# Performance work log

Measured on AMD Instinct MI355X. Metric: run time of the kernel, lower is better.

The kernel has to match this reference:

```python
import jax, jax.numpy as jnp
import numpy as np

ALPHA = 20.0 / 100.0  # dt / tau
ONE_MINUS_ALPHA = 1.0 - ALPHA


def setup_inputs() -> dict:
    key = jax.random.key(0)
    ks = jax.random.split(key, 7)
    T, B, I, H, O = 512, 256, 256, 1024, 128
    si, sh, so = 1.0 / np.sqrt(I), 1.0 / np.sqrt(H), 1.0 / np.sqrt(H)
    return {
        "x": jax.random.normal(ks[0], (T, B, I), dtype=jnp.float32),
        "Wi": jax.random.normal(ks[1], (H, I), dtype=jnp.float32) * si,
        "bi": jax.random.normal(ks[2], (H,), dtype=jnp.float32) * si,
        "Wh": jax.random.normal(ks[3], (H, H), dtype=jnp.float32) * sh,
        "bh": jax.random.normal(ks[4], (H,), dtype=jnp.float32) * sh,
        "Wo": jax.random.normal(ks[5], (O, H), dtype=jnp.float32) * so,
        "bo": jax.random.normal(ks[6], (O,), dtype=jnp.float32) * so,
    }


def reference(x, Wi, bi, Wh, bh, Wo, bo):
    T, B, I = x.shape
    H = Wh.shape[0]
    # Precompute input projection for all timesteps: [T, B, H]
    inp_proj = jnp.einsum("tbi,hi->tbh", x, Wi) + bi

    def step(carry, u_t):
        state, out = carry
        total = u_t + out @ Wh.T + bh
        state = state * ONE_MINUS_ALPHA + total * ALPHA
        out = jax.nn.relu(state)
        return (state, out), out

    init = (jnp.zeros((B, H), x.dtype), jnp.zeros((B, H), x.dtype))
    (_, _), rnn_activity = jax.lax.scan(step, init, inp_proj)  # [T, B, H]
    out = jnp.einsum("tbh,oh->tbo", rnn_activity, Wo) + bo  # [T, B, O]
    return out, rnn_activity
```

## Files before the change

### kernel.cpp

```cpp
#include <hip/hip_runtime.h>

using f4_t  = __attribute__((ext_vector_type(4))) float;
using bf8_t = __attribute__((ext_vector_type(8))) short;
using u32x4 = __attribute__((ext_vector_type(4))) unsigned int;

#define T_DIM 512
#define B_DIM 256
#define I_DIM 256
#define H_DIM 1024
#define O_DIM 128

#define SWZ(row, byte) ((byte) ^ (((row) & 7) << 4))
#define HSWZ(row, byte) ((byte) ^ (((row) & 15) << 4))

#define SMASK 0x8000800080008000ull

__device__ __forceinline__ unsigned short f2bf(float f) {
  unsigned u = __builtin_bit_cast(unsigned, f);
  return (unsigned short)((u + 0x7FFFu + ((u >> 16) & 1u)) >> 16);
}

__device__ __forceinline__ unsigned long long pack4bf(f4_t v) {
  unsigned long long r;
  r  = (unsigned long long)f2bf(v[0]);
  r |= (unsigned long long)f2bf(v[1]) << 16;
  r |= (unsigned long long)f2bf(v[2]) << 32;
  r |= (unsigned long long)f2bf(v[3]) << 48;
  return r;
}

__global__ __launch_bounds__(256, 1) void k_init(
    const float* __restrict__ Wi, const float* __restrict__ Wh,
    const float* __restrict__ Wo, unsigned short* __restrict__ Wi_b,
    unsigned short* __restrict__ Wh_b, unsigned short* __restrict__ Wo_b,
    unsigned short* __restrict__ hbuf1, unsigned* __restrict__ done) {
  int idx = blockIdx.x * 256 + threadIdx.x;
  int stride = gridDim.x * 256;
  for (int i = idx; i < H_DIM * H_DIM; i += stride) Wh_b[i] = f2bf(Wh[i]);
  for (int i = idx; i < H_DIM * I_DIM; i += stride) Wi_b[i] = f2bf(Wi[i]);
  for (int i = idx; i < O_DIM * H_DIM; i += stride) Wo_b[i] = f2bf(Wo[i]);
  for (int i = idx; i < B_DIM * H_DIM; i += stride) hbuf1[i] = 0x8000;
  for (int i = idx; i < 256 * 32; i += stride) done[i] = 0;
}

__global__ __launch_bounds__(256, 2) void k_inproj(
    const float* __restrict__ x, const unsigned short* __restrict__ Wi_b,
    const float* __restrict__ bi, float* __restrict__ act) {
  __shared__ unsigned short As[128 * 128];
  __shared__ unsigned short Bs[128 * 128];
  int blk = blockIdx.x;
  int mb = (blk & 7) * 128 + (blk >> 6);
  int nb = (blk >> 3) & 7;
  int m0 = mb * 128, n0 = nb * 128;
  int tid = threadIdx.x;
  int lane = tid & 63, w = tid >> 6;
  int wm0 = (w & 1) * 64, wn0 = (w >> 1) * 64;
  int lrow = lane & 15, lk = (lane >> 4) * 8;
  f4_t acc[4][4];
#pragma unroll
  for (int a = 0; a < 4; ++a)
#pragma unroll
    for (int b = 0; b < 4; ++b) acc[a][b] = (f4_t){0.f, 0.f, 0.f, 0.f};

  for (int kb = 0; kb < 2; ++kb) {
    if (kb) __syncthreads();
#pragma unroll
    for (int it = 0; it < 16; ++it) {
      int c = it * 256 + tid;
      int row = c >> 5;
      int kc = (c & 31) * 4;
      f4_t v = *(const f4_t*)(x + (size_t)(m0 + row) * I_DIM + kb * 128 + kc);
      *(unsigned long long*)((char*)As + SWZ(row, row * 256 + kc * 2)) = pack4bf(v);
    }
#pragma unroll
    for (int it = 0; it < 8; ++it) {
      int c = it * 256 + tid;
      int row = c >> 4;
      int k16 = c & 15;
      u32x4 v = *(const u32x4*)(Wi_b + (size_t)(n0 + row) * I_DIM + kb * 128 + k16 * 8);
      *(u32x4*)((char*)Bs + SWZ(row, row * 256 + k16 * 16)) = v;
    }
    __syncthreads();
#pragma unroll
    for (int ks = 0; ks < 4; ++ks) {
      bf8_t aF[4], bF[4];
#pragma unroll
      for (int mt = 0; mt < 4; ++mt) {
        int row = wm0 + mt * 16 + lrow;
        aF[mt] = *(const bf8_t*)((char*)As + SWZ(row, row * 256 + (ks * 32 + lk) * 2));
      }
#pragma unroll
      for (int nt = 0; nt < 4; ++nt) {
        int row = wn0 + nt * 16 + lrow;
        bF[nt] = *(const bf8_t*)((char*)Bs + SWZ(row, row * 256 + (ks * 32 + lk) * 2));
      }
#pragma unroll
      for (int mt = 0; mt < 4; ++mt)
#pragma unroll
        for (int nt = 0; nt < 4; ++nt)
          acc[mt][nt] =
              __builtin_amdgcn_mfma_f32_16x16x32_bf16(aF[mt], bF[nt], acc[mt][nt], 0, 0, 0);
    }
  }
#pragma unroll
  for (int nt = 0; nt < 4; ++nt) {
    int col = n0 + wn0 + nt * 16 + lrow;
    float bv = bi[col];
#pragma unroll
    for (int mt = 0; mt < 4; ++mt) {
      int rbase = m0 + wm0 + mt * 16 + (lane >> 4) * 4;
#pragma unroll
      for (int r = 0; r < 4; ++r)
        act[(size_t)(rbase + r) * H_DIM + col] = acc[mt][nt][r] + bv;
    }
  }
}

__global__ __launch_bounds__(512, 1) void k_scan(
    const unsigned short* __restrict__ Wh_b, const float* __restrict__ bh,
    float* __restrict__ act, unsigned short* __restrict__ hbuf0,
    unsigned short* __restrict__ hbuf1, unsigned* __restrict__ done) {
  __shared__ __align__(16) char hT[16 * 2048];
  __shared__ __align__(16) float pbuf[4][16][132];
  int blk = blockIdx.x;
  int g = blk & 15, hs = blk >> 4;
  int b0 = g * 16, h0 = hs * 128;
  int tid = threadIdx.x;
  int lane = tid & 63, w = tid >> 6;
  int nb = w & 1, ks = w >> 1;
  int lrow = lane & 15, lgq = lane >> 4;

  bf8_t Bf[4][8];
#pragma unroll
  for (int n = 0; n < 4; ++n)
#pragma unroll
    for (int kc = 0; kc < 8; ++kc)
      Bf[n][kc] = *(const bf8_t*)(Wh_b +
                                  (size_t)(h0 + nb * 64 + n * 16 + lrow) * H_DIM +
                                  ks * 256 + kc * 32 + lgq * 8);

  int pr = tid >> 5, pc = (tid & 31) * 4;
  float st[4] = {0.f, 0.f, 0.f, 0.f};
  f4_t bh4 = *(const f4_t*)(bh + h0 + pc);

  unsigned short* hb[2] = {hbuf0, hbuf1};
  unsigned* myslot = done + (g * 8 + hs) * 32;
  const unsigned* pollp = done + (g * 8 + (lane & 7)) * 32;
  bool dopoll = (lane < 8) && (lane != hs);

  f4_t ucur = *(const f4_t*)(act + (size_t)(b0 + pr) * H_DIM + h0 + pc);

  for (int t = 0; t < T_DIM; ++t) {
    int p = t & 1;
    const unsigned short* hprev = hb[p ^ 1];
    unsigned want32 = ((((unsigned)(t - 1) >> 1) & 1u) ? 0x80008000u : 0u);

    if (t > 0 && dopoll) {
      int gd = 0;
      while (__hip_atomic_load(pollp, __ATOMIC_RELAXED, __HIP_MEMORY_SCOPE_AGENT) <
                 (unsigned)t &&
             ++gd < 60000)
        __builtin_amdgcn_s_sleep(1);
    }
    __builtin_amdgcn_sched_barrier(0);

    const char* base = (const char*)(hprev + (size_t)b0 * H_DIM);
    unsigned long long a0 = (unsigned long long)(base + tid * 16);
    u32x4 q0, q1, q2, q3;
    asm volatile(
        "global_load_dwordx4 %[d0], %[a0], off sc0 sc1\n\t"
        "global_load_dwordx4 %[d1], %[a1], off sc0 sc1\n\t"
        "global_load_dwordx4 %[d2], %[a2], off sc0 sc1\n\t"
        "global_load_dwordx4 %[d3], %[a3], off sc0 sc1\n\t"
        "s_waitcnt vmcnt(0)"
        : [d0] "=&v"(q0), [d1] "=&v"(q1), [d2] "=&v"(q2), [d3] "=&v"(q3)
        : [a0] "v"(a0), [a1] "v"(a0 + 8192), [a2] "v"(a0 + 16384),
          [a3] "v"(a0 + 24576)
        : "memory");
    __builtin_amdgcn_sched_barrier(0);

    int tn = (t + 1 < T_DIM) ? t + 1 : t;
    f4_t unext = *(const f4_t*)(act + ((size_t)tn * B_DIM + b0 + pr) * H_DIM + h0 + pc);

#define STALE(qq) \
  ((((qq[0] ^ want32) | (qq[1] ^ want32) | (qq[2] ^ want32) | (qq[3] ^ want32)) & \
    0x80008000u) != 0u)
#define RELOAD(qq, ad)                                                          \
  asm volatile("global_load_dwordx4 %0, %1, off sc0 sc1\n\ts_waitcnt vmcnt(0)"  \
               : "=&v"(qq)                                                      \
               : "v"(ad)                                                        \
               : "memory")
    {
      int vg = 0;
      for (;;) {
        unsigned m = (STALE(q0) ? 1u : 0u) | (STALE(q1) ? 2u : 0u) |
                     (STALE(q2) ? 4u : 0u) | (STALE(q3) ? 8u : 0u);
        if (m == 0u || ++vg >= 400) break;
        __builtin_amdgcn_s_sleep(1);
        if (m & 1u) RELOAD(q0, a0);
        if (m & 2u) RELOAD(q1, a0 + 8192);
        if (m & 4u) RELOAD(q2, a0 + 16384);
        if (m & 8u) RELOAD(q3, a0 + 24576);
      }
    }
#undef STALE
#undef RELOAD
#pragma unroll
    for (int d = 0; d < 4; ++d) {
      q0[d] &= 0x7fff7fffu; q1[d] &= 0x7fff7fffu;
      q2[d] &= 0x7fff7fffu; q3[d] &= 0x7fff7fffu;
    }

    int rh = tid >> 7;
    int colb = (tid & 127) * 16;
#define STAGE(qq, k)                                                            \
  *(u32x4*)(&hT[((k) * 4 + rh) * 2048 + HSWZ((k) * 4 + rh, colb)]) = qq
    STAGE(q0, 0); STAGE(q1, 1); STAGE(q2, 2); STAGE(q3, 3);
#undef STAGE
    asm volatile("s_waitcnt lgkmcnt(0)\ns_barrier" ::: "memory");
    __builtin_amdgcn_sched_barrier(0);

    f4_t acc[4];
#pragma unroll
    for (int n = 0; n < 4; ++n) acc[n] = (f4_t){0.f, 0.f, 0.f, 0.f};
#pragma unroll
    for (int kc = 0; kc < 8; ++kc) {
      int cbyte = ks * 512 + kc * 64 + lgq * 16;
      bf8_t Af = *(const bf8_t*)(&hT[lrow * 2048 + HSWZ(lrow, cbyte)]);
#pragma unroll
      for (int n = 0; n < 4; ++n)
        acc[n] = __builtin_amdgcn_mfma_f32_16x16x32_bf16(Af, Bf[n][kc], acc[n], 0, 0, 0);
    }

#pragma unroll
    for (int n = 0; n < 4; ++n)
#pragma unroll
      for (int r = 0; r < 4; ++r)
        pbuf[ks][lgq * 4 + r][nb * 64 + n * 16 + lrow] = acc[n][r];
    asm volatile("s_waitcnt lgkmcnt(0)\ns_barrier" ::: "memory");
    __builtin_amdgcn_sched_barrier(0);

    f4_t s0 = *(const f4_t*)&pbuf[0][pr][pc];
    f4_t s1 = *(const f4_t*)&pbuf[1][pr][pc];
    f4_t s2 = *(const f4_t*)&pbuf[2][pr][pc];
    f4_t s3 = *(const f4_t*)&pbuf[3][pr][pc];
    f4_t tot = s0 + s1 + s2 + s3 + ucur + bh4;
    f4_t hres;
#pragma unroll
    for (int j = 0; j < 4; ++j) {
      st[j] = st[j] * 0.8f + tot[j] * 0.2f;
      hres[j] = fmaxf(st[j], 0.f);
    }

    unsigned long long hp = pack4bf(hres) | (((t >> 1) & 1) ? SMASK : 0ull);
    unsigned long long sa =
        (unsigned long long)(hb[p] + (size_t)(b0 + pr) * H_DIM + h0 + pc);
    asm volatile("global_store_dwordx2 %0, %1, off sc0 sc1" ::"v"(sa), "v"(hp)
                 : "memory");

    asm volatile("s_barrier" ::: "memory");
    if (tid == 0)
      __hip_atomic_store(myslot, (unsigned)(t + 1), __ATOMIC_RELAXED,
                         __HIP_MEMORY_SCOPE_AGENT);

    *(f4_t*)(act + ((size_t)t * B_DIM + b0 + pr) * H_DIM + h0 + pc) = hres;
    ucur = unext;
  }
}

__global__ __launch_bounds__(256, 2) void k_outproj(
    const float* __restrict__ act, const unsigned short* __restrict__ Wo_b,
    const float* __restrict__ bo, float* __restrict__ out) {
  __shared__ unsigned short As[128 * 64];
  __shared__ unsigned short Bs[128 * 64];
  int m0 = blockIdx.x * 128;
  int tid = threadIdx.x;
  int lane = tid & 63, w = tid >> 6;
  int wm0 = (w & 1) * 64, wn0 = (w >> 1) * 64;
  int lrow = lane & 15, lk = (lane >> 4) * 8;
  f4_t acc[4][4];
#pragma unroll
  for (int a = 0; a < 4; ++a)
#pragma unroll
    for (int b = 0; b < 4; ++b) acc[a][b] = (f4_t){0.f, 0.f, 0.f, 0.f};

  for (int kb = 0; kb < 16; ++kb) {
    if (kb) __syncthreads();
#pragma unroll
    for (int it = 0; it < 8; ++it) {
      int c = it * 256 + tid;
      int row = c >> 4;
      int kc = (c & 15) * 4;
      f4_t v = *(const f4_t*)(act + (size_t)(m0 + row) * H_DIM + kb * 64 + kc);
      *(unsigned long long*)((char*)As + SWZ(row, row * 128 + kc * 2)) = pack4bf(v);
    }
#pragma unroll
    for (int it = 0; it < 4; ++it) {
      int c = it * 256 + tid;
      int row = c >> 3;
      int k16 = c & 7;
      u32x4 v = *(const u32x4*)(Wo_b + (size_t)row * H_DIM + kb * 64 + k16 * 8);
      *(u32x4*)((char*)Bs + SWZ(row, row * 128 + k16 * 16)) = v;
    }
    __syncthreads();
#pragma unroll
    for (int ks = 0; ks < 2; ++ks) {
      bf8_t aF[4], bF[4];
#pragma unroll
      for (int mt = 0; mt < 4; ++mt) {
        int row = wm0 + mt * 16 + lrow;
        aF[mt] = *(const bf8_t*)((char*)As + SWZ(row, row * 128 + (ks * 32 + lk) * 2));
      }
#pragma unroll
      for (int nt = 0; nt < 4; ++nt) {
        int row = wn0 + nt * 16 + lrow;
        bF[nt] = *(const bf8_t*)((char*)Bs + SWZ(row, row * 128 + (ks * 32 + lk) * 2));
      }
#pragma unroll
      for (int mt = 0; mt < 4; ++mt)
#pragma unroll
        for (int nt = 0; nt < 4; ++nt)
          acc[mt][nt] =
              __builtin_amdgcn_mfma_f32_16x16x32_bf16(aF[mt], bF[nt], acc[mt][nt], 0, 0, 0);
    }
  }
#pragma unroll
  for (int nt = 0; nt < 4; ++nt) {
    int col = wn0 + nt * 16 + lrow;
    float bv = bo[col];
#pragma unroll
    for (int mt = 0; mt < 4; ++mt) {
      int rbase = m0 + wm0 + mt * 16 + (lane >> 4) * 4;
#pragma unroll
      for (int r = 0; r < 4; ++r)
        out[(size_t)(rbase + r) * O_DIM + col] = acc[mt][nt][r] + bv;
    }
  }
}

extern "C" void kernel_launch(void* const* d_in, const int* in_sizes, int n_in,
                              void* d_out, int out_size, void* d_ws, size_t ws_size,
                              hipStream_t stream) {
  const float* x  = (const float*)d_in[0];
  const float* Wi = (const float*)d_in[1];
  const float* bi = (const float*)d_in[2];
  const float* Wh = (const float*)d_in[3];
  const float* bh = (const float*)d_in[4];
  const float* Wo = (const float*)d_in[5];
  const float* bo = (const float*)d_in[6];

  float* out = (float*)d_out;
  float* act = out + (size_t)T_DIM * B_DIM * O_DIM;

  char* ws = (char*)d_ws;
  unsigned short* Wh_b  = (unsigned short*)(ws);
  unsigned short* Wi_b  = (unsigned short*)(ws + (2u << 20));
  unsigned short* Wo_b  = (unsigned short*)(ws + (2u << 20) + (512u << 10));
  unsigned short* hbuf0 = (unsigned short*)(ws + (2u << 20) + (768u << 10));
  unsigned short* hbuf1 = (unsigned short*)(ws + (2u << 20) + (1280u << 10));
  unsigned* done        = (unsigned*)(ws + (2u << 20) + (1792u << 10));

  k_init<<<1024, 256, 0, stream>>>(Wi, Wh, Wo, Wi_b, Wh_b, Wo_b, hbuf1, done);
  k_inproj<<<8192, 256, 0, stream>>>(x, Wi_b, bi, act);
  k_scan<<<128, 512, 0, stream>>>(Wh_b, bh, act, hbuf0, hbuf1, done);
  k_outproj<<<1024, 256, 0, stream>>>(act, Wo_b, bo, out);
}
```

Measured before the change: 1.618 ms.

## Interleave two batch groups per scan block to overlap sync latency with compute

Each scan block now owns two 16-row batch groups (A and B) and the grid is halved from 128 to 64 blocks. The loop is software-pipelined: while group A's step is being computed, group B's hidden-state loads are already in flight. Group A's next-step polling and loads are issued before group B is processed. This is meant to hide the cross-block flag polling and global-load latency of the recurrent dependency behind useful MFMA work. In exchange it doubles the LDS buffers, raises register pressure, and relies on partial vmcnt waits with store/load ordering subtleties in the final step.

```diff
diff --git a/kernel.cpp b/kernel.cpp
--- a/kernel.cpp
+++ b/kernel.cpp
@@ -120,11 +120,14 @@
     const unsigned short* __restrict__ Wh_b, const float* __restrict__ bh,
     float* __restrict__ act, unsigned short* __restrict__ hbuf0,
     unsigned short* __restrict__ hbuf1, unsigned* __restrict__ done) {
-  __shared__ __align__(16) char hT[16 * 2048];
-  __shared__ __align__(16) float pbuf[4][16][132];
+  __shared__ __align__(16) char hTA[16 * 2048];
+  __shared__ __align__(16) char hTB[16 * 2048];
+  __shared__ __align__(16) float pbufA[4][16][132];
+  __shared__ __align__(16) float pbufB[4][16][132];
   int blk = blockIdx.x;
-  int g = blk & 15, hs = blk >> 4;
-  int b0 = g * 16, h0 = hs * 128;
+  int pair = blk & 7, hs = blk >> 3;
+  int gA = pair * 2, gB = pair * 2 + 1;
+  int b0A = gA * 16, b0B = gB * 16, h0 = hs * 128;
   int tid = threadIdx.x;
   int lane = tid & 63, w = tid >> 6;
   int nb = w & 1, ks = w >> 1;
@@ -140,132 +143,152 @@
                                   ks * 256 + kc * 32 + lgq * 8);
 
   int pr = tid >> 5, pc = (tid & 31) * 4;
-  float st[4] = {0.f, 0.f, 0.f, 0.f};
+  float stA[4] = {0.f, 0.f, 0.f, 0.f};
+  float stB[4] = {0.f, 0.f, 0.f, 0.f};
   f4_t bh4 = *(const f4_t*)(bh + h0 + pc);
 
   unsigned short* hb[2] = {hbuf0, hbuf1};
-  unsigned* myslot = done + (g * 8 + hs) * 32;
-  const unsigned* pollp = done + (g * 8 + (lane & 7)) * 32;
+  unsigned* slotA = done + (gA * 8 + hs) * 32;
+  unsigned* slotB = done + (gB * 8 + hs) * 32;
+  const unsigned* pollA = done + (gA * 8 + (lane & 7)) * 32;
+  const unsigned* pollB = done + (gB * 8 + (lane & 7)) * 32;
   bool dopoll = (lane < 8) && (lane != hs);
 
-  f4_t ucur = *(const f4_t*)(act + (size_t)(b0 + pr) * H_DIM + h0 + pc);
-
-  for (int t = 0; t < T_DIM; ++t) {
-    int p = t & 1;
-    const unsigned short* hprev = hb[p ^ 1];
-    unsigned want32 = ((((unsigned)(t - 1) >> 1) & 1u) ? 0x80008000u : 0u);
-
-    if (t > 0 && dopoll) {
-      int gd = 0;
-      while (__hip_atomic_load(pollp, __ATOMIC_RELAXED, __HIP_MEMORY_SCOPE_AGENT) <
-                 (unsigned)t &&
-             ++gd < 60000)
-        __builtin_amdgcn_s_sleep(1);
-    }
-    __builtin_amdgcn_sched_barrier(0);
-
-    const char* base = (const char*)(hprev + (size_t)b0 * H_DIM);
-    unsigned long long a0 = (unsigned long long)(base + tid * 16);
-    u32x4 q0, q1, q2, q3;
-    asm volatile(
-        "global_load_dwordx4 %[d0], %[a0], off sc0 sc1\n\t"
-        "global_load_dwordx4 %[d1], %[a1], off sc0 sc1\n\t"
-        "global_load_dwordx4 %[d2], %[a2], off sc0 sc1\n\t"
-        "global_load_dwordx4 %[d3], %[a3], off sc0 sc1\n\t"
-        "s_waitcnt vmcnt(0)"
-        : [d0] "=&v"(q0), [d1] "=&v"(q1), [d2] "=&v"(q2), [d3] "=&v"(q3)
-        : [a0] "v"(a0), [a1] "v"(a0 + 8192), [a2] "v"(a0 + 16384),
-          [a3] "v"(a0 + 24576)
-        : "memory");
-    __builtin_amdgcn_sched_barrier(0);
-
-    int tn = (t + 1 < T_DIM) ? t + 1 : t;
-    f4_t unext = *(const f4_t*)(act + ((size_t)tn * B_DIM + b0 + pr) * H_DIM + h0 + pc);
-
-#define STALE(qq) \
-  ((((qq[0] ^ want32) | (qq[1] ^ want32) | (qq[2] ^ want32) | (qq[3] ^ want32)) & \
+  f4_t uA = *(const f4_t*)(act + (size_t)(b0A + pr) * H_DIM + h0 + pc);
+  f4_t uB = *(const f4_t*)(act + (size_t)(b0B + pr) * H_DIM + h0 + pc);
+
+  int rh = tid >> 7;
+  int colb = (tid & 127) * 16;
+
+  u32x4 qA0, qA1, qA2, qA3, qB0, qB1, qB2, qB3;
+  unsigned long long aA, aB;
+
+#define ISSUE4(q0_, q1_, q2_, q3_, a_)                                          \
+  asm volatile("global_load_dwordx4 %[d0], %[a0], off sc0 sc1\n\t"              \
+               "global_load_dwordx4 %[d1], %[a1], off sc0 sc1\n\t"              \
+               "global_load_dwordx4 %[d2], %[a2], off sc0 sc1\n\t"              \
+               "global_load_dwordx4 %[d3], %[a3], off sc0 sc1"                  \
+               : [d0] "=&v"(q0_), [d1] "=&v"(q1_), [d2] "=&v"(q2_),             \
+                 [d3] "=&v"(q3_)                                                \
+               : [a0] "v"(a_), [a1] "v"(a_ + 8192), [a2] "v"(a_ + 16384),       \
+                 [a3] "v"(a_ + 24576)                                           \
+               : "memory")
+#define STALEQ(qq, wnt) \
+  ((((qq[0] ^ (wnt)) | (qq[1] ^ (wnt)) | (qq[2] ^ (wnt)) | (qq[3] ^ (wnt))) & \
     0x80008000u) != 0u)
-#define RELOAD(qq, ad)                                                          \
+#define RELOADQ(qq, ad)                                                         \
   asm volatile("global_load_dwordx4 %0, %1, off sc0 sc1\n\ts_waitcnt vmcnt(0)"  \
                : "=&v"(qq)                                                      \
                : "v"(ad)                                                        \
                : "memory")
-    {
-      int vg = 0;
-      for (;;) {
-        unsigned m = (STALE(q0) ? 1u : 0u) | (STALE(q1) ? 2u : 0u) |
-                     (STALE(q2) ? 4u : 0u) | (STALE(q3) ? 8u : 0u);
-        if (m == 0u || ++vg >= 400) break;
+#define VALIDATE4(q0_, q1_, q2_, q3_, a_, wnt)                                  \
+  {                                                                             \
+    int vg = 0;                                                                 \
+    for (;;) {                                                                  \
+      unsigned m = (STALEQ(q0_, wnt) ? 1u : 0u) | (STALEQ(q1_, wnt) ? 2u : 0u) |\
+                   (STALEQ(q2_, wnt) ? 4u : 0u) | (STALEQ(q3_, wnt) ? 8u : 0u); \
+      if (m == 0u || ++vg >= 400) break;                                        \
+      __builtin_amdgcn_s_sleep(1);                                              \
+      if (m & 1u) RELOADQ(q0_, a_);                                             \
+      if (m & 2u) RELOADQ(q1_, a_ + 8192);                                      \
+      if (m & 4u) RELOADQ(q2_, a_ + 16384);                                     \
+      if (m & 8u) RELOADQ(q3_, a_ + 24576);                                     \
+    }                                                                           \
+    _Pragma("unroll") for (int d = 0; d < 4; ++d) {                             \
+      q0_[d] &= 0x7fff7fffu; q1_[d] &= 0x7fff7fffu;                             \
+      q2_[d] &= 0x7fff7fffu; q3_[d] &= 0x7fff7fffu;                             \
+    }                                                                           \
+  }
+#define PROCESS(q0_, q1_, q2_, q3_, a_, hT_, pbuf_, st_, u_, b0_, slot_, wnt)   \
+  {                                                                             \
+    asm volatile("s_waitcnt vmcnt(4)" ::: "memory");                            \
+    __builtin_amdgcn_sched_barrier(0);                                          \
+    VALIDATE4(q0_, q1_, q2_, q3_, a_, wnt);                                     \
+    *(u32x4*)(&hT_[(0 * 4 + rh) * 2048 + HSWZ(0 * 4 + rh, colb)]) = q0_;        \
+    *(u32x4*)(&hT_[(1 * 4 + rh) * 2048 + HSWZ(1 * 4 + rh, colb)]) = q1_;        \
+    *(u32x4*)(&hT_[(2 * 4 + rh) * 2048 + HSWZ(2 * 4 + rh, colb)]) = q2_;        \
+    *(u32x4*)(&hT_[(3 * 4 + rh) * 2048 + HSWZ(3 * 4 + rh, colb)]) = q3_;        \
+    asm volatile("s_waitcnt lgkmcnt(0)\ns_barrier" ::: "memory");               \
+    __builtin_amdgcn_sched_barrier(0);                                          \
+    f4_t acc[4];                                                                \
+    _Pragma("unroll") for (int n = 0; n < 4; ++n)                               \
+        acc[n] = (f4_t){0.f, 0.f, 0.f, 0.f};                                    \
+    _Pragma("unroll") for (int kc = 0; kc < 8; ++kc) {                          \
+      int cbyte = ks * 512 + kc * 64 + lgq * 16;                                \
+      bf8_t Af = *(const bf8_t*)(&hT_[lrow * 2048 + HSWZ(lrow, cbyte)]);        \
+      _Pragma("unroll") for (int n = 0; n < 4; ++n)                             \
+          acc[n] =                                                              \
+              __builtin_amdgcn_mfma_f32_16x16x32_bf16(Af, Bf[n][kc], acc[n], 0, 0, 0); \
+    }                                                                           \
+    _Pragma("unroll") for (int n = 0; n < 4; ++n) _Pragma("unroll")             \
+        for (int r = 0; r < 4; ++r)                                             \
+            pbuf_[ks][lgq * 4 + r][nb * 64 + n * 16 + lrow] = acc[n][r];        \
+    asm volatile("s_waitcnt lgkmcnt(0)\ns_barrier" ::: "memory");               \
+    __builtin_amdgcn_sched_barrier(0);                                          \
+    f4_t s0 = *(const f4_t*)&pbuf_[0][pr][pc];                                  \
+    f4_t s1 = *(const f4_t*)&pbuf_[1][pr][pc];                                  \
+    f4_t s2 = *(const f4_t*)&pbuf_[2][pr][pc];                                  \
+    f4_t s3 = *(const f4_t*)&pbuf_[3][pr][pc];                                  \
+    f4_t tot = s0 + s1 + s2 + s3 + u_ + bh4;                                    \
+    f4_t hres;                                                                  \
+    _Pragma("unroll") for (int j = 0; j < 4; ++j) {                             \
+      st_[j] = st_[j] * 0.8f + tot[j] * 0.2f;                                   \
+      hres[j] = fmaxf(st_[j], 0.f);                                             \
+    }                                                                           \
+    unsigned long long hp = pack4bf(hres) | (((t >> 1) & 1) ? SMASK : 0ull);    \
+    unsigned long long sa =                                                     \
+        (unsigned long long)(hb[p] + (size_t)(b0_ + pr) * H_DIM + h0 + pc);     \
+    asm volatile("global_store_dwordx2 %0, %1, off sc0 sc1" ::"v"(sa), "v"(hp)  \
+                 : "memory");                                                   \
+    asm volatile("s_barrier" ::: "memory");                                     \
+    if (tid == 0)                                                               \
+      __hip_atomic_store(slot_, (unsigned)(t + 1), __ATOMIC_RELAXED,            \
+                         __HIP_MEMORY_SCOPE_AGENT);                             \
+    *(f4_t*)(act + ((size_t)t * B_DIM + b0_ + pr) * H_DIM + h0 + pc) = hres;    \
+    int tn = (t + 1 < T_DIM) ? t + 1 : t;                                       \
+    u_ = *(const f4_t*)(act + ((size_t)tn * B_DIM + b0_ + pr) * H_DIM + h0 + pc); \
+  }
+
+  aA = (unsigned long long)((const char*)(hb[1] + (size_t)b0A * H_DIM) + tid * 16);
+  ISSUE4(qA0, qA1, qA2, qA3, aA);
+
+  for (int t = 0; t < T_DIM; ++t) {
+    int p = t & 1;
+    unsigned want32 = ((((unsigned)(t - 1) >> 1) & 1u) ? 0x80008000u : 0u);
+
+    if (t > 0 && dopoll) {
+      int gd = 0;
+      while (__hip_atomic_load(pollB, __ATOMIC_RELAXED, __HIP_MEMORY_SCOPE_AGENT) <
+                 (unsigned)t &&
+             ++gd < 60000)
         __builtin_amdgcn_s_sleep(1);
-        if (m & 1u) RELOAD(q0, a0);
-        if (m & 2u) RELOAD(q1, a0 + 8192);
-        if (m & 4u) RELOAD(q2, a0 + 16384);
-        if (m & 8u) RELOAD(q3, a0 + 24576);
-      }
-    }
-#undef STALE
-#undef RELOAD
-#pragma unroll
-    for (int d = 0; d < 4; ++d) {
-      q0[d] &= 0x7fff7fffu; q1[d] &= 0x7fff7fffu;
-      q2[d] &= 0x7fff7fffu; q3[d] &= 0x7fff7fffu;
-    }
-
-    int rh = tid >> 7;
-    int colb = (tid & 127) * 16;
-#define STAGE(qq, k)                                                            \
-  *(u32x4*)(&hT[((k) * 4 + rh) * 2048 + HSWZ((k) * 4 + rh, colb)]) = qq
-    STAGE(q0, 0); STAGE(q1, 1); STAGE(q2, 2); STAGE(q3, 3);
-#undef STAGE
-    asm volatile("s_waitcnt lgkmcnt(0)\ns_barrier" ::: "memory");
+    }
     __builtin_amdgcn_sched_barrier(0);
-
-    f4_t acc[4];
-#pragma unroll
-    for (int n = 0; n < 4; ++n) acc[n] = (f4_t){0.f, 0.f, 0.f, 0.f};
-#pragma unroll
-    for (int kc = 0; kc < 8; ++kc) {
-      int cbyte = ks * 512 + kc * 64 + lgq * 16;
-      bf8_t Af = *(const bf8_t*)(&hT[lrow * 2048 + HSWZ(lrow, cbyte)]);
-#pragma unroll
-      for (int n = 0; n < 4; ++n)
-        acc[n] = __builtin_amdgcn_mfma_f32_16x16x32_bf16(Af, Bf[n][kc], acc[n], 0, 0, 0);
-    }
-
-#pragma unroll
-    for (int n = 0; n < 4; ++n)
-#pragma unroll
-      for (int r = 0; r < 4; ++r)
-        pbuf[ks][lgq * 4 + r][nb * 64 + n * 16 + lrow] = acc[n][r];
-    asm volatile("s_waitcnt lgkmcnt(0)\ns_barrier" ::: "memory");
-    __builtin_amdgcn_sched_barrier(0);
-
-    f4_t s0 = *(const f4_t*)&pbuf[0][pr][pc];
-    f4_t s1 = *(const f4_t*)&pbuf[1][pr][pc];
-    f4_t s2 = *(const f4_t*)&pbuf[2][pr][pc];
-    f4_t s3 = *(const f4_t*)&pbuf[3][pr][pc];
-    f4_t tot = s0 + s1 + s2 + s3 + ucur + bh4;
-    f4_t hres;
-#pragma unroll
-    for (int j = 0; j < 4; ++j) {
-      st[j] = st[j] * 0.8f + tot[j] * 0.2f;
-      hres[j] = fmaxf(st[j], 0.f);
-    }
-
-    unsigned long long hp = pack4bf(hres) | (((t >> 1) & 1) ? SMASK : 0ull);
-    unsigned long long sa =
-        (unsigned long long)(hb[p] + (size_t)(b0 + pr) * H_DIM + h0 + pc);
-    asm volatile("global_store_dwordx2 %0, %1, off sc0 sc1" ::"v"(sa), "v"(hp)
-                 : "memory");
-
-    asm volatile("s_barrier" ::: "memory");
-    if (tid == 0)
-      __hip_atomic_store(myslot, (unsigned)(t + 1), __ATOMIC_RELAXED,
-                         __HIP_MEMORY_SCOPE_AGENT);
-
-    *(f4_t*)(act + ((size_t)t * B_DIM + b0 + pr) * H_DIM + h0 + pc) = hres;
-    ucur = unext;
-  }
+    aB = (unsigned long long)((const char*)(hb[p ^ 1] + (size_t)b0B * H_DIM) + tid * 16);
+    ISSUE4(qB0, qB1, qB2, qB3, aB);
+
+    PROCESS(qA0, qA1, qA2, qA3, aA, hTA, pbufA, stA, uA, b0A, slotA, want32);
+
+    if (t + 1 < T_DIM) {
+      if (dopoll) {
+        int gd = 0;
+        while (__hip_atomic_load(pollA, __ATOMIC_RELAXED, __HIP_MEMORY_SCOPE_AGENT) <
+                   (unsigned)(t + 1) &&
+               ++gd < 60000)
+          __builtin_amdgcn_s_sleep(1);
+      }
+      __builtin_amdgcn_sched_barrier(0);
+      aA = (unsigned long long)((const char*)(hb[p] + (size_t)b0A * H_DIM) + tid * 16);
+      ISSUE4(qA0, qA1, qA2, qA3, aA);
+    }
+
+    PROCESS(qB0, qB1, qB2, qB3, aB, hTB, pbufB, stB, uB, b0B, slotB, want32);
+  }
+#undef ISSUE4
+#undef STALEQ
+#undef RELOADQ
+#undef VALIDATE4
+#undef PROCESS
 }
 
 __global__ __launch_bounds__(256, 2) void k_outproj(
@@ -362,6 +385,6 @@
 
   k_init<<<1024, 256, 0, stream>>>(Wi, Wh, Wo, Wi_b, Wh_b, Wo_b, hbuf1, done);
   k_inproj<<<8192, 256, 0, stream>>>(x, Wi_b, bi, act);
-  k_scan<<<128, 512, 0, stream>>>(Wh_b, bh, act, hbuf0, hbuf1, done);
+  k_scan<<<64, 512, 0, stream>>>(Wh_b, bh, act, hbuf0, hbuf1, done);
   k_outproj<<<1024, 256, 0, stream>>>(act, Wo_b, bo, out);
 }
```

New measurement: 2.963 ms. 83.1% more time.

## Split recurrent scan across 256 blocks with 8-row batch groups

Applied to the files above, without the earlier changes.

The persistent scan kernel now runs 256 blocks, each owning 8 batch rows instead of 16. Each wave handles a 128-wide K slice across all 128 output columns, and the eight K-partials are summed through shared memory. This halves per-block hidden-state loads and MFMA work per step and uses more CUs. In exchange, half the MFMA rows are wasted on padding (only lgq<2 rows are written), and each step needs a larger cross-block reduction plus more polling.

```diff
diff --git a/kernel.cpp b/kernel.cpp
--- a/kernel.cpp
+++ b/kernel.cpp
@@ -1,6 +1,7 @@
 #include <hip/hip_runtime.h>
 
 using f4_t  = __attribute__((ext_vector_type(4))) float;
+using f2_t  = __attribute__((ext_vector_type(2))) float;
 using bf8_t = __attribute__((ext_vector_type(8))) short;
 using u32x4 = __attribute__((ext_vector_type(4))) unsigned int;
 
@@ -12,8 +13,6 @@
 
 #define SWZ(row, byte) ((byte) ^ (((row) & 7) << 4))
 #define HSWZ(row, byte) ((byte) ^ (((row) & 15) << 4))
-
-#define SMASK 0x8000800080008000ull
 
 __device__ __forceinline__ unsigned short f2bf(float f) {
   unsigned u = __builtin_bit_cast(unsigned, f);
@@ -40,7 +39,7 @@
   for (int i = idx; i < H_DIM * I_DIM; i += stride) Wi_b[i] = f2bf(Wi[i]);
   for (int i = idx; i < O_DIM * H_DIM; i += stride) Wo_b[i] = f2bf(Wo[i]);
   for (int i = idx; i < B_DIM * H_DIM; i += stride) hbuf1[i] = 0x8000;
-  for (int i = idx; i < 256 * 32; i += stride) done[i] = 0;
+  for (int i = idx; i < 32 * 8 * 8; i += stride) done[i] = 0;
 }
 
 __global__ __launch_bounds__(256, 2) void k_inproj(
@@ -121,34 +120,44 @@
     float* __restrict__ act, unsigned short* __restrict__ hbuf0,
     unsigned short* __restrict__ hbuf1, unsigned* __restrict__ done) {
   __shared__ __align__(16) char hT[16 * 2048];
-  __shared__ __align__(16) float pbuf[4][16][132];
+  __shared__ __align__(16) float pbuf[8][8][132];
   int blk = blockIdx.x;
-  int g = blk & 15, hs = blk >> 4;
-  int b0 = g * 16, h0 = hs * 128;
+  int g = blk & 31, s = blk >> 5;
+  int b0 = g * 8, h0 = s * 128;
   int tid = threadIdx.x;
   int lane = tid & 63, w = tid >> 6;
-  int nb = w & 1, ks = w >> 1;
   int lrow = lane & 15, lgq = lane >> 4;
 
-  bf8_t Bf[4][8];
-#pragma unroll
-  for (int n = 0; n < 4; ++n)
-#pragma unroll
-    for (int kc = 0; kc < 8; ++kc)
-      Bf[n][kc] = *(const bf8_t*)(Wh_b +
-                                  (size_t)(h0 + nb * 64 + n * 16 + lrow) * H_DIM +
-                                  ks * 256 + kc * 32 + lgq * 8);
-
-  int pr = tid >> 5, pc = (tid & 31) * 4;
-  float st[4] = {0.f, 0.f, 0.f, 0.f};
-  f4_t bh4 = *(const f4_t*)(bh + h0 + pc);
+  bf8_t Bf[8][4];
+#pragma unroll
+  for (int n = 0; n < 8; ++n)
+#pragma unroll
+    for (int kc = 0; kc < 4; ++kc)
+      Bf[n][kc] = *(const bf8_t*)(Wh_b + (size_t)(h0 + n * 16 + lrow) * H_DIM +
+                                  w * 128 + kc * 32 + lgq * 8);
+
+  int pr = tid >> 6, pc = (tid & 63) * 2;
+  float st0 = 0.f, st1 = 0.f;
+  float bhv0 = bh[h0 + pc], bhv1 = bh[h0 + pc + 1];
 
   unsigned short* hb[2] = {hbuf0, hbuf1};
-  unsigned* myslot = done + (g * 8 + hs) * 32;
-  const unsigned* pollp = done + (g * 8 + (lane & 7)) * 32;
-  bool dopoll = (lane < 8) && (lane != hs);
-
-  f4_t ucur = *(const f4_t*)(act + (size_t)(b0 + pr) * H_DIM + h0 + pc);
+  unsigned* myslot = done + (g * 8 + s) * 8;
+  const unsigned* pollp = done + (g * 8 + (lane & 7)) * 8;
+  bool dopoll = (lane < 8) && (lane != s);
+
+  f2_t ucur = *(const f2_t*)(act + (size_t)(b0 + pr) * H_DIM + h0 + pc);
+
+  int r0 = tid >> 7;
+  int colb = (tid & 127) * 16;
+
+#define RELOAD(qq, ad)                                                          \
+  asm volatile("global_load_dwordx4 %0, %1, off sc0 sc1\n\ts_waitcnt vmcnt(0)"  \
+               : "=&v"(qq)                                                      \
+               : "v"(ad)                                                        \
+               : "memory")
+#define STALE(qq) \
+  ((((qq[0] ^ want32) | (qq[1] ^ want32) | (qq[2] ^ want32) | (qq[3] ^ want32)) & \
+    0x80008000u) != 0u)
 
   for (int t = 0; t < T_DIM; ++t) {
     int p = t & 1;
@@ -166,96 +175,78 @@
 
     const char* base = (const char*)(hprev + (size_t)b0 * H_DIM);
     unsigned long long a0 = (unsigned long long)(base + tid * 16);
-    u32x4 q0, q1, q2, q3;
+    u32x4 q0, q1;
     asm volatile(
         "global_load_dwordx4 %[d0], %[a0], off sc0 sc1\n\t"
         "global_load_dwordx4 %[d1], %[a1], off sc0 sc1\n\t"
-        "global_load_dwordx4 %[d2], %[a2], off sc0 sc1\n\t"
-        "global_load_dwordx4 %[d3], %[a3], off sc0 sc1\n\t"
         "s_waitcnt vmcnt(0)"
-        : [d0] "=&v"(q0), [d1] "=&v"(q1), [d2] "=&v"(q2), [d3] "=&v"(q3)
-        : [a0] "v"(a0), [a1] "v"(a0 + 8192), [a2] "v"(a0 + 16384),
-          [a3] "v"(a0 + 24576)
+        : [d0] "=&v"(q0), [d1] "=&v"(q1)
+        : [a0] "v"(a0), [a1] "v"(a0 + 8192)
         : "memory");
     __builtin_amdgcn_sched_barrier(0);
 
     int tn = (t + 1 < T_DIM) ? t + 1 : t;
-    f4_t unext = *(const f4_t*)(act + ((size_t)tn * B_DIM + b0 + pr) * H_DIM + h0 + pc);
-
-#define STALE(qq) \
-  ((((qq[0] ^ want32) | (qq[1] ^ want32) | (qq[2] ^ want32) | (qq[3] ^ want32)) & \
-    0x80008000u) != 0u)
-#define RELOAD(qq, ad)                                                          \
-  asm volatile("global_load_dwordx4 %0, %1, off sc0 sc1\n\ts_waitcnt vmcnt(0)"  \
-               : "=&v"(qq)                                                      \
-               : "v"(ad)                                                        \
-               : "memory")
+    f2_t unext = *(const f2_t*)(act + ((size_t)tn * B_DIM + b0 + pr) * H_DIM + h0 + pc);
+
     {
       int vg = 0;
       for (;;) {
-        unsigned m = (STALE(q0) ? 1u : 0u) | (STALE(q1) ? 2u : 0u) |
-                     (STALE(q2) ? 4u : 0u) | (STALE(q3) ? 8u : 0u);
+        unsigned m = (STALE(q0) ? 1u : 0u) | (STALE(q1) ? 2u : 0u);
         if (m == 0u || ++vg >= 400) break;
         __builtin_amdgcn_s_sleep(1);
         if (m & 1u) RELOAD(q0, a0);
         if (m & 2u) RELOAD(q1, a0 + 8192);
-        if (m & 4u) RELOAD(q2, a0 + 16384);
-        if (m & 8u) RELOAD(q3, a0 + 24576);
-      }
-    }
-#undef STALE
-#undef RELOAD
+      }
+    }
 #pragma unroll
     for (int d = 0; d < 4; ++d) {
-      q0[d] &= 0x7fff7fffu; q1[d] &= 0x7fff7fffu;
-      q2[d] &= 0x7fff7fffu; q3[d] &= 0x7fff7fffu;
-    }
-
-    int rh = tid >> 7;
-    int colb = (tid & 127) * 16;
-#define STAGE(qq, k)                                                            \
-  *(u32x4*)(&hT[((k) * 4 + rh) * 2048 + HSWZ((k) * 4 + rh, colb)]) = qq
-    STAGE(q0, 0); STAGE(q1, 1); STAGE(q2, 2); STAGE(q3, 3);
-#undef STAGE
+      q0[d] &= 0x7fff7fffu;
+      q1[d] &= 0x7fff7fffu;
+    }
+
+    *(u32x4*)(&hT[r0 * 2048 + HSWZ(r0, colb)]) = q0;
+    *(u32x4*)(&hT[(r0 + 4) * 2048 + HSWZ(r0 + 4, colb)]) = q1;
     asm volatile("s_waitcnt lgkmcnt(0)\ns_barrier" ::: "memory");
     __builtin_amdgcn_sched_barrier(0);
 
-    f4_t acc[4];
-#pragma unroll
-    for (int n = 0; n < 4; ++n) acc[n] = (f4_t){0.f, 0.f, 0.f, 0.f};
-#pragma unroll
-    for (int kc = 0; kc < 8; ++kc) {
-      int cbyte = ks * 512 + kc * 64 + lgq * 16;
+    f4_t acc[8];
+#pragma unroll
+    for (int n = 0; n < 8; ++n) acc[n] = (f4_t){0.f, 0.f, 0.f, 0.f};
+#pragma unroll
+    for (int kc = 0; kc < 4; ++kc) {
+      int cbyte = w * 256 + kc * 64 + lgq * 16;
       bf8_t Af = *(const bf8_t*)(&hT[lrow * 2048 + HSWZ(lrow, cbyte)]);
 #pragma unroll
-      for (int n = 0; n < 4; ++n)
+      for (int n = 0; n < 8; ++n)
         acc[n] = __builtin_amdgcn_mfma_f32_16x16x32_bf16(Af, Bf[n][kc], acc[n], 0, 0, 0);
     }
 
-#pragma unroll
-    for (int n = 0; n < 4; ++n)
-#pragma unroll
-      for (int r = 0; r < 4; ++r)
-        pbuf[ks][lgq * 4 + r][nb * 64 + n * 16 + lrow] = acc[n][r];
+    if (lgq < 2) {
+#pragma unroll
+      for (int n = 0; n < 8; ++n)
+#pragma unroll
+        for (int r = 0; r < 4; ++r)
+          pbuf[w][lgq * 4 + r][n * 16 + lrow] = acc[n][r];
+    }
     asm volatile("s_waitcnt lgkmcnt(0)\ns_barrier" ::: "memory");
     __builtin_amdgcn_sched_barrier(0);
 
-    f4_t s0 = *(const f4_t*)&pbuf[0][pr][pc];
-    f4_t s1 = *(const f4_t*)&pbuf[1][pr][pc];
-    f4_t s2 = *(const f4_t*)&pbuf[2][pr][pc];
-    f4_t s3 = *(const f4_t*)&pbuf[3][pr][pc];
-    f4_t tot = s0 + s1 + s2 + s3 + ucur + bh4;
-    f4_t hres;
-#pragma unroll
-    for (int j = 0; j < 4; ++j) {
-      st[j] = st[j] * 0.8f + tot[j] * 0.2f;
-      hres[j] = fmaxf(st[j], 0.f);
-    }
-
-    unsigned long long hp = pack4bf(hres) | (((t >> 1) & 1) ? SMASK : 0ull);
+    float t0 = ucur[0] + bhv0, t1 = ucur[1] + bhv1;
+#pragma unroll
+    for (int k = 0; k < 8; ++k) {
+      f2_t sv = *(const f2_t*)&pbuf[k][pr][pc];
+      t0 += sv[0];
+      t1 += sv[1];
+    }
+    st0 = st0 * 0.8f + t0 * 0.2f;
+    st1 = st1 * 0.8f + t1 * 0.2f;
+    float h0v = fmaxf(st0, 0.f), h1v = fmaxf(st1, 0.f);
+
+    unsigned hp = (unsigned)f2bf(h0v) | ((unsigned)f2bf(h1v) << 16);
+    hp |= (((t >> 1) & 1) ? 0x80008000u : 0u);
     unsigned long long sa =
         (unsigned long long)(hb[p] + (size_t)(b0 + pr) * H_DIM + h0 + pc);
-    asm volatile("global_store_dwordx2 %0, %1, off sc0 sc1" ::"v"(sa), "v"(hp)
+    asm volatile("global_store_dword %0, %1, off sc0 sc1" ::"v"(sa), "v"(hp)
                  : "memory");
 
     asm volatile("s_barrier" ::: "memory");
@@ -263,9 +254,12 @@
       __hip_atomic_store(myslot, (unsigned)(t + 1), __ATOMIC_RELAXED,
                          __HIP_MEMORY_SCOPE_AGENT);
 
-    *(f4_t*)(act + ((size_t)t * B_DIM + b0 + pr) * H_DIM + h0 + pc) = hres;
+    f2_t hres2 = (f2_t){h0v, h1v};
+    *(f2_t*)(act + ((size_t)t * B_DIM + b0 + pr) * H_DIM + h0 + pc) = hres2;
     ucur = unext;
   }
+#undef RELOAD
+#undef STALE
 }
 
 __global__ __launch_bounds__(256, 2) void k_outproj(
@@ -362,6 +356,6 @@
 
   k_init<<<1024, 256, 0, stream>>>(Wi, Wh, Wo, Wi_b, Wh_b, Wo_b, hbuf1, done);
   k_inproj<<<8192, 256, 0, stream>>>(x, Wi_b, bi, act);
-  k_scan<<<128, 512, 0, stream>>>(Wh_b, bh, act, hbuf0, hbuf1, done);
+  k_scan<<<256, 512, 0, stream>>>(Wh_b, bh, act, hbuf0, hbuf1, done);
   k_outproj<<<1024, 256, 0, stream>>>(act, Wo_b, bo, out);
 }
```

After: 1.566 ms. -3.2%, faster.
